# Performance work log

Measured on AMD Instinct MI355X. Metric: run time of the kernel, lower is better.

The kernel has to match this reference:

```python
import jax, jax.numpy as jnp
import numpy as np

WS = (7, 7, 7)
N = WS[0] * WS[1] * WS[2]          # 343 tokens per window
B, D, L, H = 128, 512, 6, 8
DH = D // H                        # 64
DFF = 4 * D
EPS = 1e-5


def _relative_position_index_3d(ws):
    d = np.arange(ws[0]); h = np.arange(ws[1]); w = np.arange(ws[2])
    coords = np.stack(np.meshgrid(d, h, w, indexing='ij'))      # [3, D, H, W]
    cf = coords.reshape(3, -1)                                   # [3, n]
    rel = cf[:, :, None] - cf[:, None, :]                        # [3, n, n]
    rel = rel.transpose(1, 2, 0).copy()                          # [n, n, 3]
    rel[:, :, 0] += ws[0] - 1
    rel[:, :, 1] += ws[1] - 1
    rel[:, :, 2] += ws[2] - 1
    rel[:, :, 0] *= (2 * ws[1] - 1) * (2 * ws[2] - 1)
    rel[:, :, 1] *= 2 * ws[2] - 1
    return rel.sum(-1).astype(np.int32)                          # [n, n]


def setup_inputs() -> dict:
    key = jax.random.key(0)
    ks = jax.random.split(key, 16)
    s = lambda d: 1.0 / np.sqrt(d)
    inp = {
        'x':    jax.random.normal(ks[0], (B, N, D), jnp.float32),
        'Wq':   jax.random.normal(ks[1], (L, D, D), jnp.float32) * s(D),
        'Wk':   jax.random.normal(ks[2], (L, D, D), jnp.float32) * s(D),
        'Wv':   jax.random.normal(ks[3], (L, D, D), jnp.float32) * s(D),
        'Wo':   jax.random.normal(ks[4], (L, D, D), jnp.float32) * s(D),
        'W1ff': jax.random.normal(ks[5], (L, D, DFF), jnp.float32) * s(D),
        'b1ff': jnp.zeros((L, DFF), jnp.float32),
        'W2ff': jax.random.normal(ks[6], (L, DFF, D), jnp.float32) * s(DFF),
        'b2ff': jnp.zeros((L, D), jnp.float32),
        'ln1_g': jnp.ones((L, D), jnp.float32),
        'ln1_b': jnp.zeros((L, D), jnp.float32),
        'ln2_g': jnp.ones((L, D), jnp.float32),
        'ln2_b': jnp.zeros((L, D), jnp.float32),
        'lnf_g': jnp.ones((D,), jnp.float32),
        'lnf_b': jnp.zeros((D,), jnp.float32),
        'rel_table': jax.random.normal(ks[7], ((2 * WS[0] - 1) * (2 * WS[1] - 1) * (2 * WS[2] - 1), H), jnp.float32) * 0.02,
        'cpb_w1': jax.random.normal(ks[8], (H, 512), jnp.float32) * s(H),
        'cpb_b1': jax.random.normal(ks[9], (512,), jnp.float32) * 0.02,
        'cpb_w2': jax.random.normal(ks[10], (512, H), jnp.float32) * s(512),
        'rel_index': jnp.asarray(_relative_position_index_3d(WS)),
    }
    return inp


def _layer_norm(x, g, b):
    mu = jnp.mean(x, -1, keepdims=True)
    xc = x - mu
    var = jnp.mean(xc * xc, -1, keepdims=True)
    return xc * jax.lax.rsqrt(var + EPS) * g + b


def _rel_pos_bias(rel_table, cpb_w1, cpb_b1, cpb_w2, rel_index):
    # cpb_mlp: Linear(H->512) + ReLU + Linear(512->H, no bias)
    t = jax.nn.relu(rel_table @ cpb_w1 + cpb_b1) @ cpb_w2        # [T, H]
    bias = t[rel_index.reshape(-1)].reshape(N, N, H)             # gather -> [n, n, H]
    return jnp.transpose(bias, (2, 0, 1))                        # [H, n, n]


def reference(x, Wq, Wk, Wv, Wo, W1ff, b1ff, W2ff, b2ff,
              ln1_g, ln1_b, ln2_g, ln2_b, lnf_g, lnf_b,
              rel_table, cpb_w1, cpb_b1, cpb_w2, rel_index):
    bias = _rel_pos_bias(rel_table, cpb_w1, cpb_b1, cpb_w2, rel_index)  # [H, n, n] shared across layers
    scale = DH ** -0.5
    for l in range(L):
        # --- attention block (pre-norm) ---
        h = _layer_norm(x, ln1_g[l], ln1_b[l])
        q = (h @ Wq[l]).reshape(B, N, H, DH)
        k = (h @ Wk[l]).reshape(B, N, H, DH)
        v = (h @ Wv[l]).reshape(B, N, H, DH)
        scores = jnp.einsum('bihd,bjhd->bhij', q, k) * scale + bias[None]
        attn = jax.nn.softmax(scores, axis=-1)
        o = jnp.einsum('bhij,bjhd->bihd', attn, v).reshape(B, N, D)
        x = x + o @ Wo[l]
        # --- feed-forward block (pre-norm) ---
        h = _layer_norm(x, ln2_g[l], ln2_b[l])
        x = x + jax.nn.gelu(h @ W1ff[l] + b1ff[l]) @ W2ff[l] + b2ff[l]
    return _layer_norm(x, lnf_g, lnf_b)
```

## Files before the change

### kernel.cpp

```cpp
#include <hip/hip_runtime.h>

typedef __attribute__((ext_vector_type(8))) short short8;
typedef __attribute__((ext_vector_type(4))) float fx4;
typedef __attribute__((ext_vector_type(4))) int ix4;

#define MFMA16(a, b, c) __builtin_amdgcn_mfma_f32_16x16x32_bf16((a), (b), (c), 0, 0, 0)

__device__ __forceinline__ short f2bf(float f) {
  unsigned u = __float_as_uint(f);
  u += 0x7fffu + ((u >> 16) & 1u);
  return (short)(u >> 16);
}
__device__ __forceinline__ float bf2f(short v) {
  return __uint_as_float(((unsigned)(unsigned short)v) << 16);
}
__device__ __forceinline__ void glds16(const short* g, short* l) {
  __builtin_amdgcn_global_load_lds((const __attribute__((address_space(1))) void*)g,
                                   (__attribute__((address_space(3))) void*)l, 16, 0, 0);
}

__global__ __launch_bounds__(256)
void transpose_cvt(const float* __restrict__ W, short* __restrict__ Wt, int K, int N) {
  __shared__ float tile[64][65];
  const int kb = blockIdx.x * 64, nb = blockIdx.y * 64;
  const int t = threadIdx.x;
  const int tr = t >> 6, tc = t & 63;
#pragma unroll 4
  for (int i = 0; i < 16; i++) {
    int r = i * 4 + tr;
    tile[r][tc] = W[(size_t)(kb + r) * N + nb + tc];
  }
  __syncthreads();
#pragma unroll 4
  for (int i = 0; i < 16; i++) {
    int r = i * 4 + tr;
    Wt[(size_t)(nb + r) * K + kb + tc] = f2bf(tile[tc][r]);
  }
}

__global__ __launch_bounds__(256)
void cpb_kernel(const float* __restrict__ rt, const float* __restrict__ w1,
                const float* __restrict__ b1, const float* __restrict__ w2,
                float* __restrict__ tt) {
  const int id = blockIdx.x * 256 + threadIdx.x;
  if (id >= 2197 * 8) return;
  const int row = id >> 3, hh = id & 7;
  float r[8];
#pragma unroll
  for (int i = 0; i < 8; i++) r[i] = rt[row * 8 + i];
  float acc = 0.0f;
  for (int c = 0; c < 512; c++) {
    float s = b1[c];
#pragma unroll
    for (int i = 0; i < 8; i++) s += r[i] * w1[i * 512 + c];
    s = fmaxf(s, 0.0f);
    acc += s * w2[c * 8 + hh];
  }
  tt[id] = acc;
}

__global__ __launch_bounds__(256)
void build_biasfrag(const float* __restrict__ tt, const int* __restrict__ ridx,
                    short* __restrict__ biasb) {
  const int id = blockIdx.x * 256 + threadIdx.x;
  if (id >= 8 * 22 * 11 * 512) return;
  const int e = id & 7;
  const int lane = (id >> 3) & 63;
  const int rest = id >> 9;
  const int jp = rest % 11;
  const int rest2 = rest / 11;
  const int qt = rest2 % 22;
  const int h = rest2 / 22;
  const int q = qt * 16 + ((lane >> 4) << 2) + (e & 3);
  const int tok = (jp * 2 + (e >> 2)) * 16 + (lane & 15);
  float val = -1e30f;
  if (q < 343 && tok < 343) val = tt[ridx[q * 343 + tok] * 8 + h];
  biasb[id] = f2bf(val);
}

template <bool BF16OUT>
__global__ __launch_bounds__(256)
void ln_kernel(const float* x, const float* __restrict__ g,
               const float* __restrict__ bb, void* out) {
  const int row = blockIdx.x * 4 + (threadIdx.x >> 6);
  const int lane = threadIdx.x & 63;
  const float* xr = x + (size_t)row * 512 + lane * 8;
  fx4 va = *(const fx4*)xr;
  fx4 vb = *(const fx4*)(xr + 4);
  float s = va[0] + va[1] + va[2] + va[3] + vb[0] + vb[1] + vb[2] + vb[3];
#pragma unroll
  for (int d = 1; d < 64; d <<= 1) s += __shfl_xor(s, d);
  const float mu = s * (1.0f / 512.0f);
  float v[8];
#pragma unroll
  for (int i = 0; i < 4; i++) { v[i] = va[i] - mu; v[4 + i] = vb[i] - mu; }
  float s2 = 0.0f;
#pragma unroll
  for (int i = 0; i < 8; i++) s2 += v[i] * v[i];
#pragma unroll
  for (int d = 1; d < 64; d <<= 1) s2 += __shfl_xor(s2, d);
  const float rs = rsqrtf(s2 * (1.0f / 512.0f) + 1e-5f);
  fx4 ga = *(const fx4*)(g + lane * 8);
  fx4 gb = *(const fx4*)(g + lane * 8 + 4);
  fx4 ba = *(const fx4*)(bb + lane * 8);
  fx4 b2 = *(const fx4*)(bb + lane * 8 + 4);
  float o[8];
#pragma unroll
  for (int i = 0; i < 4; i++) {
    o[i] = v[i] * rs * ga[i] + ba[i];
    o[4 + i] = v[4 + i] * rs * gb[i] + b2[i];
  }
  if (BF16OUT) {
    short8 ov;
#pragma unroll
    for (int i = 0; i < 8; i++) ov[i] = f2bf(o[i]);
    *(short8*)((short*)out + (size_t)row * 512 + lane * 8) = ov;
  } else {
    float* op = (float*)out + (size_t)row * 512 + lane * 8;
    fx4 o1, o2;
#pragma unroll
    for (int i = 0; i < 4; i++) { o1[i] = o[i]; o2[i] = o[4 + i]; }
    *(fx4*)op = o1;
    *(fx4*)(op + 4) = o2;
  }
}

template <int EPI>
__global__ __launch_bounds__(256)
void gemm128(const short* __restrict__ A, const short* __restrict__ Bt,
             int N, int K, int nbn, int scaleN,
             const float* __restrict__ bias, const float* xres, void* out) {
  __shared__ short Al[4096];
  __shared__ short Bl[4096];
  const int nwg = gridDim.x;
  const int orig = blockIdx.x;
  const int qq = nwg >> 3, rr = nwg & 7, xc = orig & 7, o8 = orig >> 3;
  const int wgid = (xc < rr ? xc * (qq + 1) : rr * (qq + 1) + (xc - rr) * qq) + o8;
  const int m0 = (wgid / nbn) * 128, n0 = (wgid % nbn) * 128;
  const int t = threadIdx.x;
  const int lane = t & 63, wv = t >> 6;
  const int wm = (wv >> 1) * 64, wn = (wv & 1) * 64;
  const int lr = lane & 15, lg = lane >> 4;
  const int srow = wv * 32 + (lane >> 2);
  const int skk = (lane & 3) * 8;
  const short* ag0 = A + (size_t)(m0 + srow) * K + skk;
  const short* ag1 = A + (size_t)(m0 + srow + 16) * K + skk;
  const short* bg0 = Bt + (size_t)(n0 + srow) * K + skk;
  const short* bg1 = Bt + (size_t)(n0 + srow + 16) * K + skk;
  short* la0 = Al + wv * 1024;
  short* la1 = Al + wv * 1024 + 512;
  short* lb0 = Bl + wv * 1024;
  short* lb1 = Bl + wv * 1024 + 512;
  fx4 acc[4][4] = {};
  for (int kt = 0; kt < K; kt += 32) {
    glds16(ag0 + kt, la0);
    glds16(ag1 + kt, la1);
    glds16(bg0 + kt, lb0);
    glds16(bg1 + kt, lb1);
    __syncthreads();
    short8 af[4], bf[4];
#pragma unroll
    for (int i = 0; i < 4; i++) af[i] = *(const short8*)&Al[(wm + i * 16 + lr) * 32 + lg * 8];
#pragma unroll
    for (int i = 0; i < 4; i++) bf[i] = *(const short8*)&Bl[(wn + i * 16 + lr) * 32 + lg * 8];
#pragma unroll
    for (int mi = 0; mi < 4; mi++)
#pragma unroll
      for (int ni = 0; ni < 4; ni++)
        acc[mi][ni] = MFMA16(af[mi], bf[ni], acc[mi][ni]);
    __syncthreads();
  }
#pragma unroll
  for (int mi = 0; mi < 4; mi++) {
#pragma unroll
    for (int ni = 0; ni < 4; ni++) {
#pragma unroll
      for (int r = 0; r < 4; r++) {
        const int row = m0 + wm + mi * 16 + lg * 4 + r;
        const int col = n0 + wn + ni * 16 + lr;
        const float vacc = acc[mi][ni][r];
        const size_t idx = (size_t)row * N + col;
        if (EPI == 0) {
          const float sc = (col < scaleN) ? 0.125f : 1.0f;
          ((short*)out)[idx] = f2bf(vacc * sc);
        } else if (EPI == 1) {
          ((float*)out)[idx] = xres[idx] + vacc;
        } else if (EPI == 2) {
          const float v = vacc + bias[col];
          const float u = 0.7978845608f * (v + 0.044715f * v * v * v);
          ((short*)out)[idx] = f2bf(v / (1.0f + __expf(-2.0f * u)));
        } else {
          ((float*)out)[idx] = xres[idx] + vacc + bias[col];
        }
      }
    }
  }
}

__global__ __launch_bounds__(512, 1)
void attn_kernel(const short* __restrict__ qkv, const short* __restrict__ biasb,
                 short* __restrict__ obuf) {
  __shared__ short Kl[352][72];
  __shared__ short Vt[64][360];
  __shared__ short Pl[8][16][96];
  const int b = blockIdx.x >> 3, h = blockIdx.x & 7;
  const int t = threadIdx.x, lane = t & 63, wv = t >> 6;
  const int lr = lane & 15, lg = lane >> 4;
  const size_t base = (size_t)b * 343 * 1536 + h * 64;
  const short* qg = qkv + base;
  const short* kg = qkv + base + 512;
  const short* vg = qkv + base + 1024;
  for (int c = t; c < 352 * 8; c += 512) {
    const int tok = c >> 3, d8 = (c & 7) * 8;
    const int ts = tok < 343 ? tok : 342;
    short8 kvv = *(const short8*)(kg + (size_t)ts * 1536 + d8);
    short8 vvv = *(const short8*)(vg + (size_t)ts * 1536 + d8);
    *(short8*)&Kl[tok][d8] = kvv;
#pragma unroll
    for (int j = 0; j < 8; j++) Vt[d8 + j][tok] = vvv[j];
  }
  __syncthreads();
  for (int qt = wv; qt < 22; qt += 8) {
    const int q0 = qt * 16;
    const int qr = q0 + lr;
    const int qs = qr < 343 ? qr : 342;
    short8 qf0 = *(const short8*)(qg + (size_t)qs * 1536 + lg * 8);
    short8 qf1 = *(const short8*)(qg + (size_t)qs * 1536 + 32 + lg * 8);
    fx4 s[22];
#pragma unroll
    for (int j = 0; j < 22; j++) {
      short8 kf0 = *(const short8*)&Kl[j * 16 + lr][lg * 8];
      short8 kf1 = *(const short8*)&Kl[j * 16 + lr][32 + lg * 8];
      fx4 z = {0.0f, 0.0f, 0.0f, 0.0f};
      z = MFMA16(qf0, kf0, z);
      z = MFMA16(qf1, kf1, z);
      s[j] = z;
    }
    const short* bp = biasb + (size_t)((h * 22 + qt) * 11) * 512 + lane * 8;
#pragma unroll
    for (int jp = 0; jp < 11; jp++) {
      short8 bb = *(const short8*)(bp + jp * 512);
#pragma unroll
      for (int r = 0; r < 4; r++) {
        s[2 * jp][r] += bf2f(bb[r]);
        s[2 * jp + 1][r] += bf2f(bb[4 + r]);
      }
    }
    float mx[4] = {-1e30f, -1e30f, -1e30f, -1e30f};
#pragma unroll
    for (int j = 0; j < 22; j++)
#pragma unroll
      for (int r = 0; r < 4; r++) mx[r] = fmaxf(mx[r], s[j][r]);
#pragma unroll
    for (int r = 0; r < 4; r++) {
      float m = mx[r];
      m = fmaxf(m, __shfl_xor(m, 1));
      m = fmaxf(m, __shfl_xor(m, 2));
      m = fmaxf(m, __shfl_xor(m, 4));
      m = fmaxf(m, __shfl_xor(m, 8));
      mx[r] = m;
    }
    float sm[4] = {0.0f, 0.0f, 0.0f, 0.0f};
#pragma unroll
    for (int j = 0; j < 22; j++)
#pragma unroll
      for (int r = 0; r < 4; r++) {
        const float p = __expf(s[j][r] - mx[r]);
        s[j][r] = p;
        sm[r] += p;
      }
#pragma unroll
    for (int r = 0; r < 4; r++) {
      float ss = sm[r];
      ss += __shfl_xor(ss, 1);
      ss += __shfl_xor(ss, 2);
      ss += __shfl_xor(ss, 4);
      ss += __shfl_xor(ss, 8);
      sm[r] = 1.0f / ss;
    }
    fx4 oacc[4] = {};
#pragma unroll
    for (int c = 0; c < 4; c++) {
      const int nj = (c < 3) ? 6 : 4;
#pragma unroll
      for (int j = 0; j < 6; j++) {
        if (j < nj) {
#pragma unroll
          for (int r = 0; r < 4; r++)
            Pl[wv][lg * 4 + r][j * 16 + lr] = f2bf(s[c * 6 + j][r] * sm[r]);
        }
      }
      const int nk = (c < 3) ? 3 : 2;
#pragma unroll
      for (int ks = 0; ks < 3; ks++) {
        if (ks < nk) {
          short8 pb = *(const short8*)&Pl[wv][lr][ks * 32 + lg * 8];
#pragma unroll
          for (int mi = 0; mi < 4; mi++) {
            short8 vva = *(const short8*)&Vt[mi * 16 + lr][c * 96 + ks * 32 + lg * 8];
            oacc[mi] = MFMA16(vva, pb, oacc[mi]);
          }
        }
      }
    }
    if (qr < 343) {
#pragma unroll
      for (int mi = 0; mi < 4; mi++)
#pragma unroll
        for (int r = 0; r < 4; r++) {
          const int dh = mi * 16 + lg * 4 + r;
          obuf[(size_t)(b * 343 + qr) * 512 + h * 64 + dh] = f2bf(oacc[mi][r]);
        }
    }
  }
}

extern "C" void kernel_launch(void* const* d_in, const int* in_sizes, int n_in,
                              void* d_out, int out_size, void* d_ws, size_t ws_size,
                              hipStream_t stream) {
  const float* x_in = (const float*)d_in[0];
  const float* Wq = (const float*)d_in[1];
  const float* Wk = (const float*)d_in[2];
  const float* Wv = (const float*)d_in[3];
  const float* Wo = (const float*)d_in[4];
  const float* W1 = (const float*)d_in[5];
  const float* b1 = (const float*)d_in[6];
  const float* W2 = (const float*)d_in[7];
  const float* b2 = (const float*)d_in[8];
  const float* ln1g = (const float*)d_in[9];
  const float* ln1b = (const float*)d_in[10];
  const float* ln2g = (const float*)d_in[11];
  const float* ln2b = (const float*)d_in[12];
  const float* lnfg = (const float*)d_in[13];
  const float* lnfb = (const float*)d_in[14];
  const float* rtab = (const float*)d_in[15];
  const float* cw1 = (const float*)d_in[16];
  const float* cb1 = (const float*)d_in[17];
  const float* cw2 = (const float*)d_in[18];
  const int* ridx = (const int*)d_in[19];
  float* xout = (float*)d_out;

  char* p = (char*)d_ws;
  short* wt = (short*)p;      p += 37748736;
  short* hbuf = (short*)p;    p += 44957696;
  char* big = p;              p += 179830784;
  short* biasb = (short*)p;   p += 1982464;
  float* tt = (float*)p;      p += 70304;
  short* qkvbuf = (short*)big;
  short* obuf = (short*)(big + 134873088);
  short* mid = (short*)big;

  cpb_kernel<<<(2197 * 8 + 255) / 256, 256, 0, stream>>>(rtab, cw1, cb1, cw2, tt);
  build_biasfrag<<<(8 * 22 * 11 * 512 + 255) / 256, 256, 0, stream>>>(tt, ridx, biasb);

  for (int l = 0; l < 6; l++) {
    const size_t wl = (size_t)l * 3145728;
    transpose_cvt<<<dim3(8, 8), 256, 0, stream>>>(Wq + (size_t)l * 262144, wt + wl, 512, 512);
    transpose_cvt<<<dim3(8, 8), 256, 0, stream>>>(Wk + (size_t)l * 262144, wt + wl + 262144, 512, 512);
    transpose_cvt<<<dim3(8, 8), 256, 0, stream>>>(Wv + (size_t)l * 262144, wt + wl + 524288, 512, 512);
    transpose_cvt<<<dim3(8, 8), 256, 0, stream>>>(Wo + (size_t)l * 262144, wt + wl + 786432, 512, 512);
    transpose_cvt<<<dim3(8, 32), 256, 0, stream>>>(W1 + (size_t)l * 1048576, wt + wl + 1048576, 512, 2048);
    transpose_cvt<<<dim3(32, 8), 256, 0, stream>>>(W2 + (size_t)l * 1048576, wt + wl + 2097152, 2048, 512);
  }

  for (int l = 0; l < 6; l++) {
    const size_t wl = (size_t)l * 3145728;
    const float* xsrc = (l == 0) ? x_in : xout;
    ln_kernel<true><<<10976, 256, 0, stream>>>(xsrc, ln1g + l * 512, ln1b + l * 512, hbuf);
    gemm128<0><<<343 * 12, 256, 0, stream>>>(hbuf, wt + wl, 1536, 512, 12, 512, nullptr, nullptr, qkvbuf);
    attn_kernel<<<1024, 512, 0, stream>>>(qkvbuf, biasb, obuf);
    gemm128<1><<<343 * 4, 256, 0, stream>>>(obuf, wt + wl + 786432, 512, 512, 4, 0, nullptr, xsrc, xout);
    ln_kernel<true><<<10976, 256, 0, stream>>>(xout, ln2g + l * 512, ln2b + l * 512, hbuf);
    gemm128<2><<<343 * 16, 256, 0, stream>>>(hbuf, wt + wl + 1048576, 2048, 512, 16, 0, b1 + l * 2048, nullptr, mid);
    gemm128<3><<<343 * 4, 256, 0, stream>>>(mid, wt + wl + 2097152, 512, 2048, 4, 0, b2 + l * 512, xout, xout);
  }
  ln_kernel<false><<<10976, 256, 0, stream>>>(xout, lnfg, lnfb, xout);
}
```

Before: 4.728 ms.

## Double-buffer GEMM LDS tiles and simplify GELU epilogue math

The bf16 GEMM main loop now uses two LDS buffers. It issues the global-to-LDS loads for the next K tile before computing on the current one, so memory latency can overlap the MFMA work, and it drops one barrier per iteration. The tanh-GELU epilogue is rewritten with folded constants, an FMA and a hardware reciprocal instead of a division. LDS usage per block doubles, which may reduce occupancy. With only one barrier, correctness depends on the async global_load_lds writes being complete at that barrier. The reciprocal is approximate.

```diff
diff --git a/kernel.cpp b/kernel.cpp
--- a/kernel.cpp
+++ b/kernel.cpp
@@ -130,8 +130,8 @@
 void gemm128(const short* __restrict__ A, const short* __restrict__ Bt,
              int N, int K, int nbn, int scaleN,
              const float* __restrict__ bias, const float* xres, void* out) {
-  __shared__ short Al[4096];
-  __shared__ short Bl[4096];
+  __shared__ short Al[8192];
+  __shared__ short Bl[8192];
   const int nwg = gridDim.x;
   const int orig = blockIdx.x;
   const int qq = nwg >> 3, rr = nwg & 7, xc = orig & 7, o8 = orig >> 3;
@@ -147,29 +147,39 @@
   const short* ag1 = A + (size_t)(m0 + srow + 16) * K + skk;
   const short* bg0 = Bt + (size_t)(n0 + srow) * K + skk;
   const short* bg1 = Bt + (size_t)(n0 + srow + 16) * K + skk;
-  short* la0 = Al + wv * 1024;
-  short* la1 = Al + wv * 1024 + 512;
-  short* lb0 = Bl + wv * 1024;
-  short* lb1 = Bl + wv * 1024 + 512;
+  const int nkt = K >> 5;
   fx4 acc[4][4] = {};
-  for (int kt = 0; kt < K; kt += 32) {
-    glds16(ag0 + kt, la0);
-    glds16(ag1 + kt, la1);
-    glds16(bg0 + kt, lb0);
-    glds16(bg1 + kt, lb1);
-    __syncthreads();
+#define STAGE(KT, BUF)                                   \
+  do {                                                   \
+    const int off_ = (KT) * 32;                          \
+    short* la_ = Al + (BUF) * 4096 + wv * 1024;          \
+    short* lb_ = Bl + (BUF) * 4096 + wv * 1024;          \
+    glds16(ag0 + off_, la_);                             \
+    glds16(ag1 + off_, la_ + 512);                       \
+    glds16(bg0 + off_, lb_);                             \
+    glds16(bg1 + off_, lb_ + 512);                       \
+  } while (0)
+  STAGE(0, 0);
+  __syncthreads();
+  int buf = 0;
+  for (int kt = 0; kt < nkt; kt++) {
+    if (kt + 1 < nkt) STAGE(kt + 1, buf ^ 1);
     short8 af[4], bf[4];
 #pragma unroll
-    for (int i = 0; i < 4; i++) af[i] = *(const short8*)&Al[(wm + i * 16 + lr) * 32 + lg * 8];
-#pragma unroll
-    for (int i = 0; i < 4; i++) bf[i] = *(const short8*)&Bl[(wn + i * 16 + lr) * 32 + lg * 8];
+    for (int i = 0; i < 4; i++)
+      af[i] = *(const short8*)&Al[buf * 4096 + (wm + i * 16 + lr) * 32 + lg * 8];
+#pragma unroll
+    for (int i = 0; i < 4; i++)
+      bf[i] = *(const short8*)&Bl[buf * 4096 + (wn + i * 16 + lr) * 32 + lg * 8];
 #pragma unroll
     for (int mi = 0; mi < 4; mi++)
 #pragma unroll
       for (int ni = 0; ni < 4; ni++)
         acc[mi][ni] = MFMA16(af[mi], bf[ni], acc[mi][ni]);
     __syncthreads();
-  }
+    buf ^= 1;
+  }
+#undef STAGE
 #pragma unroll
   for (int mi = 0; mi < 4; mi++) {
 #pragma unroll
@@ -187,8 +197,10 @@
           ((float*)out)[idx] = xres[idx] + vacc;
         } else if (EPI == 2) {
           const float v = vacc + bias[col];
-          const float u = 0.7978845608f * (v + 0.044715f * v * v * v);
-          ((short*)out)[idx] = f2bf(v / (1.0f + __expf(-2.0f * u)));
+          const float tt = v * v;
+          const float u2 = v * fmaf(tt, -0.0713548165f, -1.5957691216f);
+          const float g = v * __builtin_amdgcn_rcpf(1.0f + __expf(u2));
+          ((short*)out)[idx] = f2bf(g);
         } else {
           ((float*)out)[idx] = xres[idx] + vacc + bias[col];
         }
```

Result: faster. 4.254 ms (-10.0%).
